# Performance work log

Measured on AMD Instinct MI355X. Metric: run time of the kernel, lower is better.

## Reference

```python
import jax, jax.numpy as jnp
import numpy as np

ORDER = 4


def setup_inputs() -> dict:
    key = jax.random.key(0)
    k1, k2, k3, k4 = jax.random.split(key, 4)
    B, IN, OUT = 8192, 1024, 1024
    x = jax.random.normal(k1, (B, IN), dtype=jnp.float32)
    base_weight = jax.random.normal(k2, (OUT, IN), dtype=jnp.float32) * (1.0 / np.sqrt(IN))
    std = 1.0 / (IN * np.sqrt(ORDER))
    taylor_coeffs = jax.random.normal(k3, (OUT, IN, ORDER), dtype=jnp.float32) * std
    bound = 1.0 / np.sqrt(IN)
    bias = jax.random.uniform(k4, (OUT,), dtype=jnp.float32, minval=-bound, maxval=bound)
    return {"x": x, "base_weight": base_weight, "taylor_coeffs": taylor_coeffs, "bias": bias}


def reference(x, base_weight, taylor_coeffs, bias):
    # base path: SiLU(x) @ W^T
    base_out = jnp.einsum('bi,oi->bo', jax.nn.silu(x), base_weight)
    # taylor path: x_powers[b,i,k] = x**k, k=0..ORDER-1; contract with coeffs[o,i,k]
    powers = jnp.arange(ORDER, dtype=x.dtype)  # [K]
    x_powers = x[:, :, None] ** powers  # [B, IN, K]
    taylor_out = jnp.einsum('bik,oik->bo', x_powers, taylor_coeffs)
    return base_out + taylor_out + bias
```

## Files before the change

### kernel.cpp

```cpp
#include <hip/hip_runtime.h>
#include <hip/hip_bf16.h>

#define GLOBAL_AS __attribute__((address_space(1)))
#define LDS_AS    __attribute__((address_space(3)))

typedef __bf16 bf16x8 __attribute__((ext_vector_type(8)));
typedef float  f32x4  __attribute__((ext_vector_type(4)));

constexpr int BATCH = 8192;
constexpr int IN    = 1024;
constexpr int OUT   = 1024;
constexpr int KDIM  = IN * 4;
constexpr int TM = 128, TN = 128, BK = 64;
constexpr int NKT = KDIM / BK;

__device__ __forceinline__ unsigned short f2bf(float f) {
    union { float f; unsigned u; } v; v.f = f;
    unsigned r = v.u + 0x7fffu + ((v.u >> 16) & 1u);
    return (unsigned short)(r >> 16);
}
__device__ __forceinline__ unsigned pk(unsigned short a, unsigned short b) {
    return (unsigned)a | ((unsigned)b << 16);
}

__global__ __launch_bounds__(256) void prep(const float* __restrict__ x,
                                            const float* __restrict__ W,
                                            const float* __restrict__ C,
                                            const float* __restrict__ bias,
                                            unsigned short* __restrict__ Ab,
                                            unsigned short* __restrict__ Bb,
                                            float* __restrict__ be) {
    if (blockIdx.x < 8192) {
        int idx = blockIdx.x * 256 + threadIdx.x;
        float4 v = reinterpret_cast<const float4*>(x)[idx];
        float e0[4] = {v.x, v.y, v.z, v.w};
        unsigned short o[16];
#pragma unroll
        for (int j = 0; j < 4; ++j) {
            float xv = e0[j];
            float s  = xv / (1.0f + __expf(-xv));
            float x2 = xv * xv;
            o[4*j+0] = f2bf(s);
            o[4*j+1] = f2bf(xv);
            o[4*j+2] = f2bf(x2);
            o[4*j+3] = f2bf(x2 * xv);
        }
        uint4 d0 = make_uint4(pk(o[0],o[1]), pk(o[2],o[3]),   pk(o[4],o[5]),   pk(o[6],o[7]));
        uint4 d1 = make_uint4(pk(o[8],o[9]), pk(o[10],o[11]), pk(o[12],o[13]), pk(o[14],o[15]));
        uint4* dst = reinterpret_cast<uint4*>(Ab) + (size_t)idx * 2;
        dst[0] = d0;
        dst[1] = d1;
    } else {
        const int o = blockIdx.x - 8192, t = threadIdx.x;
        const int i0 = t * 4;
        const float4* c4 = reinterpret_cast<const float4*>(C + ((size_t)o * IN + i0) * 4);
        float4 w4 = *reinterpret_cast<const float4*>(W + (size_t)o * IN + i0);
        float wv[4] = {w4.x, w4.y, w4.z, w4.w};
        float s = 0.f;
        unsigned d[8];
#pragma unroll
        for (int j = 0; j < 4; ++j) {
            float4 c = c4[j];
            s += c.x;
            d[2*j]   = pk(f2bf(wv[j]), f2bf(c.y));
            d[2*j+1] = pk(f2bf(c.z),   f2bf(c.w));
        }
        uint4* dst = reinterpret_cast<uint4*>(Bb + (size_t)o * KDIM + i0 * 4);
        dst[0] = make_uint4(d[0], d[1], d[2], d[3]);
        dst[1] = make_uint4(d[4], d[5], d[6], d[7]);
#pragma unroll
        for (int off = 32; off > 0; off >>= 1) s += __shfl_down(s, off, 64);
        __shared__ float red[4];
        if ((t & 63) == 0) red[t >> 6] = s;
        __syncthreads();
        if (t == 0) be[o] = bias[o] + red[0] + red[1] + red[2] + red[3];
    }
}

__global__ __launch_bounds__(256, 2) void gemm_kan(
        const unsigned short* __restrict__ Ab,
        const unsigned short* __restrict__ Bb,
        const float* __restrict__ be,
        float* __restrict__ out) {
    __shared__ unsigned short sA[2][TM * BK];
    __shared__ unsigned short sB[2][TN * BK];

    const int t   = threadIdx.x;
    const int l   = blockIdx.x;
    const int bm  = (l & 7) * 8 + ((l >> 3) & 7);
    const int bn  = l >> 6;
    const int lane = t & 63;
    const int wave = t >> 6;
    const int wr   = wave >> 1;
    const int wc   = wave & 1;
    const int l15  = lane & 15;
    const int quad = lane >> 4;

    const int rowT = t >> 3;
    const int gT   = (t & 7) ^ (rowT & 7);
    const unsigned short* pa[4];
    const unsigned short* pb[4];
#pragma unroll
    for (int i = 0; i < 4; ++i) {
        pa[i] = Ab + (size_t)(bm * TM + i * 32 + rowT) * KDIM + gT * 8;
        pb[i] = Bb + (size_t)(bn * TN + i * 32 + rowT) * KDIM + gT * 8;
    }

    f32x4 acc[4][4];
    const f32x4 zero = {0.f, 0.f, 0.f, 0.f};
#pragma unroll
    for (int i = 0; i < 4; ++i)
#pragma unroll
        for (int j = 0; j < 4; ++j) acc[i][j] = zero;

    const int xr = l15 & 7;

#pragma unroll
    for (int i = 0; i < 4; ++i) {
        __builtin_amdgcn_global_load_lds((const GLOBAL_AS void*)pa[i],
                                         (LDS_AS void*)(sA[0] + i * 2048 + t * 8), 16, 0, 0);
        __builtin_amdgcn_global_load_lds((const GLOBAL_AS void*)pb[i],
                                         (LDS_AS void*)(sB[0] + i * 2048 + t * 8), 16, 0, 0);
    }

    for (int kt = 0; kt < NKT; ++kt) {
        __syncthreads();

        if (kt + 1 < NKT) {
            const int koff = (kt + 1) * BK;
            const int nb = (kt + 1) & 1;
#pragma unroll
            for (int i = 0; i < 4; ++i) {
                __builtin_amdgcn_global_load_lds((const GLOBAL_AS void*)(pa[i] + koff),
                                                 (LDS_AS void*)(sA[nb] + i * 2048 + t * 8), 16, 0, 0);
                __builtin_amdgcn_global_load_lds((const GLOBAL_AS void*)(pb[i] + koff),
                                                 (LDS_AS void*)(sB[nb] + i * 2048 + t * 8), 16, 0, 0);
            }
        }

        const unsigned short* a_base = sA[kt & 1];
        const unsigned short* b_base = sB[kt & 1];
#pragma unroll
        for (int kk = 0; kk < 2; ++kk) {
            const int cq = ((kk * 4 + quad) ^ xr) * 8;
            bf16x8 af[4], bv[4];
#pragma unroll
            for (int mi = 0; mi < 4; ++mi)
                af[mi] = *reinterpret_cast<const bf16x8*>(
                    a_base + (wr * 64 + mi * 16 + l15) * BK + cq);
#pragma unroll
            for (int ni = 0; ni < 4; ++ni)
                bv[ni] = *reinterpret_cast<const bf16x8*>(
                    b_base + (wc * 64 + ni * 16 + l15) * BK + cq);
#pragma unroll
            for (int mi = 0; mi < 4; ++mi)
#pragma unroll
                for (int ni = 0; ni < 4; ++ni)
                    acc[mi][ni] = __builtin_amdgcn_mfma_f32_16x16x32_bf16(
                        af[mi], bv[ni], acc[mi][ni], 0, 0, 0);
        }
    }

    float bev[4];
#pragma unroll
    for (int ni = 0; ni < 4; ++ni)
        bev[ni] = be[bn * TN + wc * 64 + ni * 16 + l15];

#pragma unroll
    for (int mi = 0; mi < 4; ++mi) {
        const int grow = bm * TM + wr * 64 + mi * 16 + quad * 4;
#pragma unroll
        for (int ni = 0; ni < 4; ++ni) {
            const int gcol = bn * TN + wc * 64 + ni * 16 + l15;
            float* po = out + (size_t)grow * OUT + gcol;
#pragma unroll
            for (int r = 0; r < 4; ++r)
                po[(size_t)r * OUT] = acc[mi][ni][r] + bev[ni];
        }
    }
}

extern "C" void kernel_launch(void* const* d_in, const int* in_sizes, int n_in,
                              void* d_out, int out_size, void* d_ws, size_t ws_size,
                              hipStream_t stream) {
    const float* x    = (const float*)d_in[0];
    const float* W    = (const float*)d_in[1];
    const float* C    = (const float*)d_in[2];
    const float* bias = (const float*)d_in[3];
    float* out = (float*)d_out;

    unsigned short* Ab = (unsigned short*)d_ws;
    unsigned short* Bb = Ab + (size_t)BATCH * KDIM;
    float*          be = (float*)(Bb + (size_t)OUT * KDIM);

    prep<<<dim3(8192 + 1024), dim3(256), 0, stream>>>(x, W, C, bias, Ab, Bb, be);

    gemm_kan<<<dim3(512), dim3(256), 0, stream>>>(Ab, Bb, be, out);
}
```

Before: 175.5 us.

## Widen GEMM tile to 128x256 with BK=32 and use fast reciprocal in SiLU

Enlarges the output tile along N to 256, halves the K step to 32, and reworks the LDS swizzle and load mapping for the new 32-wide rows. Each wave now computes a 64x128 sub-tile, so every A fragment is reused across more MFMAs and global traffic per flop drops. The grid shrinks to 256 blocks with launch bounds of one block per SM, which leaves some of the 256 CUs idle and doubles the number of barrier-separated K iterations. SiLU in the prep kernel swaps the divide for a hardware reciprocal.

```diff
diff --git a/kernel.cpp b/kernel.cpp
--- a/kernel.cpp
+++ b/kernel.cpp
@@ -11,7 +11,7 @@
 constexpr int IN    = 1024;
 constexpr int OUT   = 1024;
 constexpr int KDIM  = IN * 4;
-constexpr int TM = 128, TN = 128, BK = 64;
+constexpr int TM = 128, TN = 256, BK = 32;
 constexpr int NKT = KDIM / BK;
 
 __device__ __forceinline__ unsigned short f2bf(float f) {
@@ -38,7 +38,7 @@
 #pragma unroll
         for (int j = 0; j < 4; ++j) {
             float xv = e0[j];
-            float s  = xv / (1.0f + __expf(-xv));
+            float s  = xv * __builtin_amdgcn_rcpf(1.0f + __expf(-xv));
             float x2 = xv * xv;
             o[4*j+0] = f2bf(s);
             o[4*j+1] = f2bf(xv);
@@ -77,7 +77,7 @@
     }
 }
 
-__global__ __launch_bounds__(256, 2) void gemm_kan(
+__global__ __launch_bounds__(256, 1) void gemm_kan(
         const unsigned short* __restrict__ Ab,
         const unsigned short* __restrict__ Bb,
         const float* __restrict__ be,
@@ -96,32 +96,37 @@
     const int l15  = lane & 15;
     const int quad = lane >> 4;
 
-    const int rowT = t >> 3;
-    const int gT   = (t & 7) ^ (rowT & 7);
-    const unsigned short* pa[4];
+    const int rowS = t >> 2;
+    const int colS = ((t & 3) ^ ((t >> 3) & 3)) * 8;
+
+    const unsigned short* pa[2];
     const unsigned short* pb[4];
 #pragma unroll
-    for (int i = 0; i < 4; ++i) {
-        pa[i] = Ab + (size_t)(bm * TM + i * 32 + rowT) * KDIM + gT * 8;
-        pb[i] = Bb + (size_t)(bn * TN + i * 32 + rowT) * KDIM + gT * 8;
-    }
-
-    f32x4 acc[4][4];
+    for (int i = 0; i < 2; ++i)
+        pa[i] = Ab + (size_t)(bm * TM + i * 64 + rowS) * KDIM + colS;
+#pragma unroll
+    for (int i = 0; i < 4; ++i)
+        pb[i] = Bb + (size_t)(bn * TN + i * 64 + rowS) * KDIM + colS;
+
+    f32x4 acc[4][8];
     const f32x4 zero = {0.f, 0.f, 0.f, 0.f};
 #pragma unroll
     for (int i = 0; i < 4; ++i)
 #pragma unroll
-        for (int j = 0; j < 4; ++j) acc[i][j] = zero;
-
-    const int xr = l15 & 7;
-
-#pragma unroll
-    for (int i = 0; i < 4; ++i) {
+        for (int j = 0; j < 8; ++j) acc[i][j] = zero;
+
+    const int xq   = (quad ^ ((l15 >> 1) & 3)) * 8;
+    const int aoff = (wr * 64 + l15) * BK + xq;
+    const int boff = (wc * 128 + l15) * BK + xq;
+
+#pragma unroll
+    for (int i = 0; i < 2; ++i)
         __builtin_amdgcn_global_load_lds((const GLOBAL_AS void*)pa[i],
                                          (LDS_AS void*)(sA[0] + i * 2048 + t * 8), 16, 0, 0);
+#pragma unroll
+    for (int i = 0; i < 4; ++i)
         __builtin_amdgcn_global_load_lds((const GLOBAL_AS void*)pb[i],
                                          (LDS_AS void*)(sB[0] + i * 2048 + t * 8), 16, 0, 0);
-    }
 
     for (int kt = 0; kt < NKT; ++kt) {
         __syncthreads();
@@ -130,48 +135,44 @@
             const int koff = (kt + 1) * BK;
             const int nb = (kt + 1) & 1;
 #pragma unroll
-            for (int i = 0; i < 4; ++i) {
+            for (int i = 0; i < 2; ++i)
                 __builtin_amdgcn_global_load_lds((const GLOBAL_AS void*)(pa[i] + koff),
                                                  (LDS_AS void*)(sA[nb] + i * 2048 + t * 8), 16, 0, 0);
+#pragma unroll
+            for (int i = 0; i < 4; ++i)
                 __builtin_amdgcn_global_load_lds((const GLOBAL_AS void*)(pb[i] + koff),
                                                  (LDS_AS void*)(sB[nb] + i * 2048 + t * 8), 16, 0, 0);
-            }
         }
 
         const unsigned short* a_base = sA[kt & 1];
         const unsigned short* b_base = sB[kt & 1];
-#pragma unroll
-        for (int kk = 0; kk < 2; ++kk) {
-            const int cq = ((kk * 4 + quad) ^ xr) * 8;
-            bf16x8 af[4], bv[4];
-#pragma unroll
-            for (int mi = 0; mi < 4; ++mi)
-                af[mi] = *reinterpret_cast<const bf16x8*>(
-                    a_base + (wr * 64 + mi * 16 + l15) * BK + cq);
-#pragma unroll
-            for (int ni = 0; ni < 4; ++ni)
-                bv[ni] = *reinterpret_cast<const bf16x8*>(
-                    b_base + (wc * 64 + ni * 16 + l15) * BK + cq);
-#pragma unroll
-            for (int mi = 0; mi < 4; ++mi)
-#pragma unroll
-                for (int ni = 0; ni < 4; ++ni)
-                    acc[mi][ni] = __builtin_amdgcn_mfma_f32_16x16x32_bf16(
-                        af[mi], bv[ni], acc[mi][ni], 0, 0, 0);
-        }
+        bf16x8 af[4], bv[8];
+#pragma unroll
+        for (int mi = 0; mi < 4; ++mi)
+            af[mi] = *reinterpret_cast<const bf16x8*>(a_base + aoff + mi * 16 * BK);
+#pragma unroll
+        for (int ni = 0; ni < 8; ++ni)
+            bv[ni] = *reinterpret_cast<const bf16x8*>(b_base + boff + ni * 16 * BK);
+
+#pragma unroll
+        for (int mi = 0; mi < 4; ++mi)
+#pragma unroll
+            for (int ni = 0; ni < 8; ++ni)
+                acc[mi][ni] = __builtin_amdgcn_mfma_f32_16x16x32_bf16(
+                    af[mi], bv[ni], acc[mi][ni], 0, 0, 0);
     }
 
-    float bev[4];
-#pragma unroll
-    for (int ni = 0; ni < 4; ++ni)
-        bev[ni] = be[bn * TN + wc * 64 + ni * 16 + l15];
+    float bev[8];
+#pragma unroll
+    for (int ni = 0; ni < 8; ++ni)
+        bev[ni] = be[bn * TN + wc * 128 + ni * 16 + l15];
 
 #pragma unroll
     for (int mi = 0; mi < 4; ++mi) {
         const int grow = bm * TM + wr * 64 + mi * 16 + quad * 4;
 #pragma unroll
-        for (int ni = 0; ni < 4; ++ni) {
-            const int gcol = bn * TN + wc * 64 + ni * 16 + l15;
+        for (int ni = 0; ni < 8; ++ni) {
+            const int gcol = bn * TN + wc * 128 + ni * 16 + l15;
             float* po = out + (size_t)grow * OUT + gcol;
 #pragma unroll
             for (int r = 0; r < 4; ++r)
@@ -195,5 +196,5 @@
 
     prep<<<dim3(8192 + 1024), dim3(256), 0, stream>>>(x, W, C, bias, Ab, Bb, be);
 
-    gemm_kan<<<dim3(512), dim3(256), 0, stream>>>(Ab, Bb, be, out);
-}
+    gemm_kan<<<dim3(256), dim3(256), 0, stream>>>(Ab, Bb, be, out);
+}
```

New measurement: 264.5 us. +50.7%, slower.

## Fuse activation feature expansion into GEMM A-tile loading from raw x

Applied to the files above, without the earlier changes.

Removes the separate pass that expanded x into a bf16 [B, 4*IN] feature matrix. The GEMM now reads fp32 x directly, computes SiLU, x, x^2 and x^3 in registers, and writes the swizzled bf16 A tile into LDS while the next x chunk is prefetched. This cuts the global write and re-read of the 64MB expanded activation matrix. The cost is that each N-block recomputes the expansion (8 times redundantly), and the A-tile path now uses register loads and LDS stores instead of async global-to-LDS copies, which can hurt overlap with the MFMA loop.

```diff
diff --git a/kernel.cpp b/kernel.cpp
--- a/kernel.cpp
+++ b/kernel.cpp
@@ -22,63 +22,42 @@
 __device__ __forceinline__ unsigned pk(unsigned short a, unsigned short b) {
     return (unsigned)a | ((unsigned)b << 16);
 }
-
-__global__ __launch_bounds__(256) void prep(const float* __restrict__ x,
-                                            const float* __restrict__ W,
-                                            const float* __restrict__ C,
-                                            const float* __restrict__ bias,
-                                            unsigned short* __restrict__ Ab,
-                                            unsigned short* __restrict__ Bb,
-                                            float* __restrict__ be) {
-    if (blockIdx.x < 8192) {
-        int idx = blockIdx.x * 256 + threadIdx.x;
-        float4 v = reinterpret_cast<const float4*>(x)[idx];
-        float e0[4] = {v.x, v.y, v.z, v.w};
-        unsigned short o[16];
-#pragma unroll
-        for (int j = 0; j < 4; ++j) {
-            float xv = e0[j];
-            float s  = xv / (1.0f + __expf(-xv));
-            float x2 = xv * xv;
-            o[4*j+0] = f2bf(s);
-            o[4*j+1] = f2bf(xv);
-            o[4*j+2] = f2bf(x2);
-            o[4*j+3] = f2bf(x2 * xv);
-        }
-        uint4 d0 = make_uint4(pk(o[0],o[1]), pk(o[2],o[3]),   pk(o[4],o[5]),   pk(o[6],o[7]));
-        uint4 d1 = make_uint4(pk(o[8],o[9]), pk(o[10],o[11]), pk(o[12],o[13]), pk(o[14],o[15]));
-        uint4* dst = reinterpret_cast<uint4*>(Ab) + (size_t)idx * 2;
-        dst[0] = d0;
-        dst[1] = d1;
-    } else {
-        const int o = blockIdx.x - 8192, t = threadIdx.x;
-        const int i0 = t * 4;
-        const float4* c4 = reinterpret_cast<const float4*>(C + ((size_t)o * IN + i0) * 4);
-        float4 w4 = *reinterpret_cast<const float4*>(W + (size_t)o * IN + i0);
-        float wv[4] = {w4.x, w4.y, w4.z, w4.w};
-        float s = 0.f;
-        unsigned d[8];
-#pragma unroll
-        for (int j = 0; j < 4; ++j) {
-            float4 c = c4[j];
-            s += c.x;
-            d[2*j]   = pk(f2bf(wv[j]), f2bf(c.y));
-            d[2*j+1] = pk(f2bf(c.z),   f2bf(c.w));
-        }
-        uint4* dst = reinterpret_cast<uint4*>(Bb + (size_t)o * KDIM + i0 * 4);
-        dst[0] = make_uint4(d[0], d[1], d[2], d[3]);
-        dst[1] = make_uint4(d[4], d[5], d[6], d[7]);
-#pragma unroll
-        for (int off = 32; off > 0; off >>= 1) s += __shfl_down(s, off, 64);
-        __shared__ float red[4];
-        if ((t & 63) == 0) red[t >> 6] = s;
-        __syncthreads();
-        if (t == 0) be[o] = bias[o] + red[0] + red[1] + red[2] + red[3];
-    }
+__device__ __forceinline__ unsigned pk2f(float a, float b) {
+    return pk(f2bf(a), f2bf(b));
+}
+
+__global__ __launch_bounds__(256) void prep_w(const float* __restrict__ W,
+                                              const float* __restrict__ C,
+                                              const float* __restrict__ bias,
+                                              unsigned short* __restrict__ Bb,
+                                              float* __restrict__ be) {
+    const int o = blockIdx.x, t = threadIdx.x;
+    const int i0 = t * 4;
+    const float4* c4 = reinterpret_cast<const float4*>(C + ((size_t)o * IN + i0) * 4);
+    float4 w4 = *reinterpret_cast<const float4*>(W + (size_t)o * IN + i0);
+    float wv[4] = {w4.x, w4.y, w4.z, w4.w};
+    float s = 0.f;
+    unsigned d[8];
+#pragma unroll
+    for (int j = 0; j < 4; ++j) {
+        float4 c = c4[j];
+        s += c.x;
+        d[2*j]   = pk2f(wv[j], c.y);
+        d[2*j+1] = pk2f(c.z,   c.w);
+    }
+    uint4* dst = reinterpret_cast<uint4*>(Bb + (size_t)o * KDIM + i0 * 4);
+    dst[0] = make_uint4(d[0], d[1], d[2], d[3]);
+    dst[1] = make_uint4(d[4], d[5], d[6], d[7]);
+#pragma unroll
+    for (int off = 32; off > 0; off >>= 1) s += __shfl_down(s, off, 64);
+    __shared__ float red[4];
+    if ((t & 63) == 0) red[t >> 6] = s;
+    __syncthreads();
+    if (t == 0) be[o] = bias[o] + red[0] + red[1] + red[2] + red[3];
 }
 
 __global__ __launch_bounds__(256, 2) void gemm_kan(
-        const unsigned short* __restrict__ Ab,
+        const float* __restrict__ x,
         const unsigned short* __restrict__ Bb,
         const float* __restrict__ be,
         float* __restrict__ out) {
@@ -96,15 +75,20 @@
     const int l15  = lane & 15;
     const int quad = lane >> 4;
 
+    const int rA = t >> 1;
+    const int hA = t & 1;
+    const float* pxt = x + (size_t)(bm * TM + rA) * IN + hA * 8;
+    unsigned aw[4];
+#pragma unroll
+    for (int jj = 0; jj < 4; ++jj)
+        aw[jj] = rA * (BK * 2) + (((4 * hA + jj) ^ (rA & 7)) * 16);
+
     const int rowT = t >> 3;
     const int gT   = (t & 7) ^ (rowT & 7);
-    const unsigned short* pa[4];
     const unsigned short* pb[4];
 #pragma unroll
-    for (int i = 0; i < 4; ++i) {
-        pa[i] = Ab + (size_t)(bm * TM + i * 32 + rowT) * KDIM + gT * 8;
+    for (int i = 0; i < 4; ++i)
         pb[i] = Bb + (size_t)(bn * TN + i * 32 + rowT) * KDIM + gT * 8;
-    }
 
     f32x4 acc[4][4];
     const f32x4 zero = {0.f, 0.f, 0.f, 0.f};
@@ -115,26 +99,52 @@
 
     const int xr = l15 & 7;
 
-#pragma unroll
-    for (int i = 0; i < 4; ++i) {
-        __builtin_amdgcn_global_load_lds((const GLOBAL_AS void*)pa[i],
-                                         (LDS_AS void*)(sA[0] + i * 2048 + t * 8), 16, 0, 0);
+    float4 x0a = *reinterpret_cast<const float4*>(pxt);
+    float4 x0b = *reinterpret_cast<const float4*>(pxt + 4);
+#pragma unroll
+    for (int i = 0; i < 4; ++i)
         __builtin_amdgcn_global_load_lds((const GLOBAL_AS void*)pb[i],
                                          (LDS_AS void*)(sB[0] + i * 2048 + t * 8), 16, 0, 0);
-    }
+    {
+        float xs[8] = {x0a.x, x0a.y, x0a.z, x0a.w, x0b.x, x0b.y, x0b.z, x0b.w};
+#pragma unroll
+        for (int jj = 0; jj < 4; ++jj) {
+            float u = xs[2*jj], v = xs[2*jj+1];
+            float su = u * __builtin_amdgcn_rcpf(1.0f + __expf(-u));
+            float sv = v * __builtin_amdgcn_rcpf(1.0f + __expf(-v));
+            float u2 = u * u, v2 = v * v;
+            uint4 d = make_uint4(pk2f(su, u), pk2f(u2, u2 * u),
+                                 pk2f(sv, v), pk2f(v2, v2 * v));
+            *reinterpret_cast<uint4*>(reinterpret_cast<char*>(sA[0]) + aw[jj]) = d;
+        }
+    }
+    float4 xna = *reinterpret_cast<const float4*>(pxt + 16);
+    float4 xnb = *reinterpret_cast<const float4*>(pxt + 20);
 
     for (int kt = 0; kt < NKT; ++kt) {
         __syncthreads();
 
+        const int nb = (kt + 1) & 1;
         if (kt + 1 < NKT) {
             const int koff = (kt + 1) * BK;
-            const int nb = (kt + 1) & 1;
-#pragma unroll
-            for (int i = 0; i < 4; ++i) {
-                __builtin_amdgcn_global_load_lds((const GLOBAL_AS void*)(pa[i] + koff),
-                                                 (LDS_AS void*)(sA[nb] + i * 2048 + t * 8), 16, 0, 0);
+#pragma unroll
+            for (int i = 0; i < 4; ++i)
                 __builtin_amdgcn_global_load_lds((const GLOBAL_AS void*)(pb[i] + koff),
                                                  (LDS_AS void*)(sB[nb] + i * 2048 + t * 8), 16, 0, 0);
+            float xs[8] = {xna.x, xna.y, xna.z, xna.w, xnb.x, xnb.y, xnb.z, xnb.w};
+#pragma unroll
+            for (int jj = 0; jj < 4; ++jj) {
+                float u = xs[2*jj], v = xs[2*jj+1];
+                float su = u * __builtin_amdgcn_rcpf(1.0f + __expf(-u));
+                float sv = v * __builtin_amdgcn_rcpf(1.0f + __expf(-v));
+                float u2 = u * u, v2 = v * v;
+                uint4 d = make_uint4(pk2f(su, u), pk2f(u2, u2 * u),
+                                     pk2f(sv, v), pk2f(v2, v2 * v));
+                *reinterpret_cast<uint4*>(reinterpret_cast<char*>(sA[nb]) + aw[jj]) = d;
+            }
+            if (kt + 2 < NKT) {
+                xna = *reinterpret_cast<const float4*>(pxt + (kt + 2) * 16);
+                xnb = *reinterpret_cast<const float4*>(pxt + (kt + 2) * 16 + 4);
             }
         }
 
@@ -189,11 +199,10 @@
     const float* bias = (const float*)d_in[3];
     float* out = (float*)d_out;
 
-    unsigned short* Ab = (unsigned short*)d_ws;
-    unsigned short* Bb = Ab + (size_t)BATCH * KDIM;
+    unsigned short* Bb = (unsigned short*)d_ws;
     float*          be = (float*)(Bb + (size_t)OUT * KDIM);
 
-    prep<<<dim3(8192 + 1024), dim3(256), 0, stream>>>(x, W, C, bias, Ab, Bb, be);
-
-    gemm_kan<<<dim3(512), dim3(256), 0, stream>>>(Ab, Bb, be, out);
-}
+    prep_w<<<dim3(OUT), dim3(256), 0, stream>>>(W, C, bias, Bb, be);
+
+    gemm_kan<<<dim3(512), dim3(256), 0, stream>>>(x, Bb, be, out);
+}
```

After: 181.5 us. +3.4%, slower.
